# Kernel tuning notes

Hardware: AMD Instinct MI355X
Metric: run time of the kernel (lower is better)

The kernel has to match this reference:

```python
import jax, jax.numpy as jnp
import numpy as np


def setup_inputs() -> dict:
    key = jax.random.key(0)
    ks = jax.random.split(key, 6)
    N, E, F, H, HOP = 100000, 1600000, 128, 128, 3
    x = jax.random.normal(ks[0], (N, F), dtype=jnp.float32)
    edge_index = jax.random.randint(ks[1], (2, E), 0, N, dtype=jnp.int64)
    # per-hop weights, scaled like nn.Linear default init magnitude
    W1 = jax.random.normal(ks[2], (HOP, H, F), dtype=jnp.float32) * (1.0 / np.sqrt(F))
    W2 = jax.random.normal(ks[3], (HOP, H, H), dtype=jnp.float32) * (1.0 / np.sqrt(H))
    W3 = jax.random.normal(ks[4], (HOP, H, H), dtype=jnp.float32) * (1.0 / np.sqrt(H))
    W4 = jax.random.normal(ks[5], (HOP, H, 1), dtype=jnp.float32)
    return {"x": x, "edge_index": edge_index, "W1": W1, "W2": W2, "W3": W3, "W4": W4}


def reference(x, edge_index, W1, W2, W3, W4):
    N = x.shape[0]
    E = edge_index.shape[1]
    H = W1.shape[1]
    hop = W1.shape[0]
    row, col = edge_index[0], edge_index[1]
    edge_attr = jnp.ones((E, 1), dtype=x.dtype)  # as in original forward
    h = jnp.zeros((N, H), dtype=x.dtype)  # initial node_embedding
    for i in range(hop):
        node_feat = x @ W1[i].T                                   # [N,H]
        # gather neighbor embeddings then scatter-sum to destination nodes
        nbr_agg = jax.ops.segment_sum(h[col], row, num_segments=N)  # [N,H]
        edge_emb = jax.nn.relu(edge_attr @ W4[i].T)               # [E,H]
        edge_agg = jax.ops.segment_sum(edge_emb, row, num_segments=N)  # [N,H]
        h = jax.nn.relu(node_feat + nbr_agg @ W2[i].T + edge_agg @ W3[i].T)
        # dropout is identity in eval mode
    return h
```

## Files before the change

### kernel.cpp

```cpp
#include <hip/hip_runtime.h>

#define H 128
#define BSH 9
#define BROWS (1 << BSH)
#define BCAP 10240

typedef __attribute__((ext_vector_type(8))) short bf16x8;
typedef __attribute__((ext_vector_type(4))) float f32x4;
typedef unsigned int uint;
typedef unsigned short ushort;

__device__ __forceinline__ ushort f2bf(float f) {
    uint u = __builtin_bit_cast(uint, f);
    uint r = u + 0x7FFFu + ((u >> 16) & 1u);
    return (ushort)(r >> 16);
}
__device__ __forceinline__ float bf_lo(uint u) {
    return __builtin_bit_cast(float, u << 16);
}
__device__ __forceinline__ float bf_hi(uint u) {
    return __builtin_bit_cast(float, u & 0xFFFF0000u);
}


__global__ void scatter_direct(const int* __restrict__ ei, int E, int NB,
                               int* __restrict__ gcnt, int2* __restrict__ ebuf) {
    __shared__ int cnt[1024];
    __shared__ int base[1024];
    int blk = blockIdx.x, t = threadIdx.x;
    for (int b = t; b < NB; b += 256) cnt[b] = 0;
    __syncthreads();
    int lo = blk << 12, hi = min(lo + 4096, E);
    for (int e = lo + t; e < hi; e += 256) atomicAdd(&cnt[ei[e] >> BSH], 1);
    __syncthreads();
    for (int b = t; b < NB; b += 256) {
        int c = cnt[b];
        base[b] = c ? atomicAdd(&gcnt[b * 16], c) : 0;
        cnt[b] = 0;
    }
    __syncthreads();
    for (int e = lo + t; e < hi; e += 256) {
        int r = ei[e], c = ei[E + e];
        int b = r >> BSH;
        int pos = base[b] + atomicAdd(&cnt[b], 1);
        if (pos < BCAP) ebuf[(size_t)b * BCAP + pos] = make_int2(r, c);
    }
}

__global__ __launch_bounds__(512)
void bucket_csr2(const int2* __restrict__ ebuf, const int* __restrict__ gcnt,
                 int NB, int N, int* __restrict__ deg, int* __restrict__ off,
                 int* __restrict__ colss) {
    __shared__ int rcnt[BROWS], rloff[BROWS];
    int b = blockIdx.x, t = threadIdx.x;
    int rowbase = b << BSH;
    int ebase = b * BCAP;
    int ne = min(gcnt[b * 16], BCAP);
    rcnt[t] = 0;
    __syncthreads();
    for (int e = t; e < ne; e += 512) atomicAdd(&rcnt[ebuf[(size_t)ebase + e].x - rowbase], 1);
    __syncthreads();
    int v = rcnt[t];
    rloff[t] = v;
    __syncthreads();
    for (int d = 1; d < BROWS; d <<= 1) {
        int u = (t >= d) ? rloff[t - d] : 0;
        __syncthreads();
        rloff[t] += u;
        __syncthreads();
    }
    int ex = rloff[t] - v;
    int row = rowbase + t;
    if (row < N) {
        deg[row] = v;
        off[row] = ebase + ex;
    }
    __syncthreads();
    rloff[t] = ex;
    rcnt[t] = 0;
    __syncthreads();
    for (int e = t; e < ne; e += 512) {
        int2 rc = ebuf[(size_t)ebase + e];
        int lr = rc.x - rowbase;
        int pz = atomicAdd(&rcnt[lr], 1);
        colss[ebase + rloff[lr] + pz] = rc.y;
    }
}


__global__ void cvec_kernel(const float* __restrict__ W3, const float* __restrict__ W4,
                            float* __restrict__ cvec) {
    __shared__ float r4[H];
    int i = blockIdx.x, t = threadIdx.x;
    if (t < H) r4[t] = fmaxf(W4[i * H + t], 0.f);
    __syncthreads();
    int wv = t >> 6, l = t & 63;
    for (int k = wv; k < H; k += 4) {
        const float* w3 = W3 + (size_t)i * H * H + (size_t)k * H;
        float s = w3[l] * r4[l] + w3[l + 64] * r4[l + 64];
        for (int d = 1; d < 64; d <<= 1) s += __shfl_xor(s, d);
        if (l == 0) cvec[i * H + k] = s;
    }
}

__global__ void cast_w(const float* __restrict__ W1, const float* __restrict__ W2,
                       ushort* __restrict__ outp, int n8) {
    int i = blockIdx.x * blockDim.x + threadIdx.x;
    if (i >= 2 * n8) return;
    const float4* in4 = (const float4*)((i < n8) ? W1 : W2);
    int j = (i < n8) ? i : i - n8;
    float4 a = in4[2 * j], b = in4[2 * j + 1];
    uint4 o;
    o.x = (uint)f2bf(a.x) | ((uint)f2bf(a.y) << 16);
    o.y = (uint)f2bf(a.z) | ((uint)f2bf(a.w) << 16);
    o.z = (uint)f2bf(b.x) | ((uint)f2bf(b.y) << 16);
    o.w = (uint)f2bf(b.z) | ((uint)f2bf(b.w) << 16);
    ((uint4*)outp)[i] = o;
}


template<int RELU, int OUT_BF16, int CAST0>
__global__ __launch_bounds__(512)
void gemm_pairs(const void* __restrict__ A0, const ushort* __restrict__ W0,
                const ushort* __restrict__ A1, const ushort* __restrict__ W1p,
                int npairs, const int* __restrict__ deg, const float* __restrict__ cvec,
                void* __restrict__ Cout, ushort* __restrict__ xbout, int N)
{
    __shared__ uint4 A4[2048];
    __shared__ uint4 W4[1024];
    int t = threadIdx.x;
    int w = t >> 6, l = t & 63;
    int lg = l >> 4, lr = l & 15;
    int rowBase = blockIdx.x * 256;

    f32x4 acc[2][8];
#pragma unroll
    for (int rt = 0; rt < 2; ++rt)
#pragma unroll
        for (int ct = 0; ct < 8; ++ct) acc[rt][ct] = (f32x4){0.f, 0.f, 0.f, 0.f};

    for (int pr = 0; pr < npairs; ++pr) {
        const uint4* Ag = (const uint4*)(pr ? (const void*)A1 : A0);
        const uint4* Wg = (const uint4*)(pr ? W1p : W0);
        for (int kc = 0; kc < 2; ++kc) {
            if (pr || kc) __syncthreads();
#pragma unroll
            for (int it = 0; it < 4; ++it) {
                int idx = it * 512 + t;
                int r = idx >> 3, s = idx & 7;
                int gr = rowBase + r;
                uint4 v = make_uint4(0, 0, 0, 0);
                if (CAST0 && pr == 0) {
                    if (gr < N) {
                        const float4* xg = (const float4*)A0;
                        float4 a = xg[(size_t)gr * 32 + (kc * 8 + s) * 2];
                        float4 b = xg[(size_t)gr * 32 + (kc * 8 + s) * 2 + 1];
                        v.x = (uint)f2bf(a.x) | ((uint)f2bf(a.y) << 16);
                        v.y = (uint)f2bf(a.z) | ((uint)f2bf(a.w) << 16);
                        v.z = (uint)f2bf(b.x) | ((uint)f2bf(b.y) << 16);
                        v.w = (uint)f2bf(b.z) | ((uint)f2bf(b.w) << 16);
                        ((uint4*)xbout)[(size_t)gr * 16 + kc * 8 + s] = v;
                    }
                } else {
                    if (gr < N) v = Ag[(size_t)gr * 16 + kc * 8 + s];
                }
                A4[r * 8 + (s ^ (r & 7))] = v;
            }
#pragma unroll
            for (int it = 0; it < 2; ++it) {
                int idx = it * 512 + t;
                int r = idx >> 3, s = idx & 7;
                W4[r * 8 + (s ^ (r & 7))] = Wg[r * 16 + kc * 8 + s];
            }
            __syncthreads();
#pragma unroll
            for (int kk = 0; kk < 2; ++kk) {
                int slot = kk * 4 + lg;
                bf16x8 af[2], bfr[8];
#pragma unroll
                for (int rt = 0; rt < 2; ++rt) {
                    int r = w * 32 + rt * 16 + lr;
                    af[rt] = *(const bf16x8*)&A4[r * 8 + (slot ^ (r & 7))];
                }
#pragma unroll
                for (int ct = 0; ct < 8; ++ct) {
                    int r = ct * 16 + lr;
                    bfr[ct] = *(const bf16x8*)&W4[r * 8 + (slot ^ (r & 7))];
                }
#pragma unroll
                for (int rt = 0; rt < 2; ++rt)
#pragma unroll
                    for (int ct = 0; ct < 8; ++ct)
                        acc[rt][ct] = __builtin_amdgcn_mfma_f32_16x16x32_bf16(
                            af[rt], bfr[ct], acc[rt][ct], 0, 0, 0);
            }
        }
    }

    float cv[8];
#pragma unroll
    for (int ct = 0; ct < 8; ++ct) cv[ct] = cvec[ct * 16 + lr];
#pragma unroll
    for (int rt = 0; rt < 2; ++rt) {
#pragma unroll
        for (int j = 0; j < 4; ++j) {
            int gr = rowBase + w * 32 + rt * 16 + lg * 4 + j;
            if (gr < N) {
                float d = (float)deg[gr];
#pragma unroll
                for (int ct = 0; ct < 8; ++ct) {
                    int gc = ct * 16 + lr;
                    float v = acc[rt][ct][j] + d * cv[ct];
                    if (RELU) v = fmaxf(v, 0.f);
                    if (OUT_BF16) ((ushort*)Cout)[(size_t)gr * H + gc] = f2bf(v);
                    else ((float*)Cout)[(size_t)gr * H + gc] = v;
                }
            }
        }
    }
}


__global__ void aggregate_sum(const ushort* __restrict__ hsrc,
                              const int* __restrict__ off, const int* __restrict__ deg,
                              const int* __restrict__ cols,
                              ushort* __restrict__ sdst, int N)
{
    int node = blockIdx.x * 4 + (threadIdx.x >> 6);
    if (node >= N) return;
    int l = threadIdx.x & 63;
    int s = off[node], e = s + deg[node];
    const uint* pu = (const uint*)hsrc;
    float ax = 0.f, ay = 0.f;
    int i = s;
    for (; i + 8 <= e; i += 8) {
        uint v0 = pu[(size_t)cols[i]     * 64 + l];
        uint v1 = pu[(size_t)cols[i + 1] * 64 + l];
        uint v2 = pu[(size_t)cols[i + 2] * 64 + l];
        uint v3 = pu[(size_t)cols[i + 3] * 64 + l];
        uint v4 = pu[(size_t)cols[i + 4] * 64 + l];
        uint v5 = pu[(size_t)cols[i + 5] * 64 + l];
        uint v6 = pu[(size_t)cols[i + 6] * 64 + l];
        uint v7 = pu[(size_t)cols[i + 7] * 64 + l];
        ax += bf_lo(v0) + bf_lo(v1) + bf_lo(v2) + bf_lo(v3)
            + bf_lo(v4) + bf_lo(v5) + bf_lo(v6) + bf_lo(v7);
        ay += bf_hi(v0) + bf_hi(v1) + bf_hi(v2) + bf_hi(v3)
            + bf_hi(v4) + bf_hi(v5) + bf_hi(v6) + bf_hi(v7);
    }
    for (; i + 4 <= e; i += 4) {
        uint v0 = pu[(size_t)cols[i]     * 64 + l];
        uint v1 = pu[(size_t)cols[i + 1] * 64 + l];
        uint v2 = pu[(size_t)cols[i + 2] * 64 + l];
        uint v3 = pu[(size_t)cols[i + 3] * 64 + l];
        ax += bf_lo(v0) + bf_lo(v1) + bf_lo(v2) + bf_lo(v3);
        ay += bf_hi(v0) + bf_hi(v1) + bf_hi(v2) + bf_hi(v3);
    }
    for (; i < e; ++i) {
        uint v = pu[(size_t)cols[i] * 64 + l];
        ax += bf_lo(v);
        ay += bf_hi(v);
    }
    ((uint*)sdst)[(size_t)node * 64 + l] = (uint)f2bf(ax) | ((uint)f2bf(ay) << 16);
}


extern "C" void kernel_launch(void* const* d_in, const int* in_sizes, int n_in,
                              void* d_out, int out_size, void* d_ws, size_t ws_size,
                              hipStream_t stream)
{
    const float* x  = (const float*)d_in[0];
    const int*   ei = (const int*)d_in[1];
    const float* W1 = (const float*)d_in[2];
    const float* W2 = (const float*)d_in[3];
    const float* W3 = (const float*)d_in[4];
    const float* W4 = (const float*)d_in[5];
    int N   = in_sizes[0] / H;
    int E   = in_sizes[1] / 2;
    int HOP = in_sizes[2] / (H * H);

    int NB   = (N + BROWS - 1) >> BSH;
    int NBLK = (E + 4095) >> 12;

    char* ws = (char*)d_ws;
    int*   gcnt  = (int*)ws;
    int*   deg   = gcnt + NB * 16;
    int*   off   = deg + N;
    int*   colss = off + N;
    float* cvec  = (float*)(colss + (size_t)NB * BCAP);
    size_t fo = (((size_t)((char*)(cvec + HOP * H) - ws)) + 255) & ~(size_t)255;
    int2*  ebuf  = (int2*)(ws + fo);
    ushort* W1b  = (ushort*)(ebuf + (size_t)NB * BCAP);
    ushort* W2b  = W1b + (size_t)HOP * H * H;
    ushort* xb   = W2b + (size_t)HOP * H * H;
    ushort* h    = xb + (size_t)N * H;
    ushort* sagg = h + (size_t)N * H;

    hipMemsetAsync(gcnt, 0, sizeof(int) * NB * 16, stream);
    scatter_direct<<<NBLK, 256, 0, stream>>>(ei, E, NB, gcnt, ebuf);
    bucket_csr2<<<NB, 512, 0, stream>>>(ebuf, gcnt, NB, N, deg, off, colss);

    cvec_kernel<<<HOP, 256, 0, stream>>>(W3, W4, cvec);

    int nw8 = HOP * H * H / 8;
    cast_w<<<(2 * nw8 + 255) / 256, 256, 0, stream>>>(W1, W2, W1b, nw8);

    int gblocks = (N + 255) / 256;
    float* out = (float*)d_out;

    if (HOP == 1) {
        gemm_pairs<1, 0, 1><<<gblocks, 512, 0, stream>>>(x, W1b, nullptr, nullptr, 1,
                                                         deg, cvec, out, xb, N);
        return;
    }
    gemm_pairs<1, 1, 1><<<gblocks, 512, 0, stream>>>(x, W1b, nullptr, nullptr, 1,
                                                     deg, cvec, h, xb, N);

    for (int i = 1; i < HOP; ++i) {
        int last = (i == HOP - 1);
        aggregate_sum<<<(N + 3) / 4, 256, 0, stream>>>(h, off, deg, colss, sagg, N);
        if (last)
            gemm_pairs<1, 0, 0><<<gblocks, 512, 0, stream>>>(xb, W1b + (size_t)i * H * H,
                                                             sagg, W2b + (size_t)i * H * H,
                                                             2, deg, cvec + i * H, out,
                                                             nullptr, N);
        else
            gemm_pairs<1, 1, 0><<<gblocks, 512, 0, stream>>>(xb, W1b + (size_t)i * H * H,
                                                             sagg, W2b + (size_t)i * H * H,
                                                             2, deg, cvec + i * H, h,
                                                             nullptr, N);
    }
}
```

Measured before the change: 262.7 us.

## Gather hop-1 neighbor embeddings in FP8 and enlarge CSR buckets

Adds a cast kernel that quantizes the bf16 hidden state to FP8 (scaled by 1/8, clamped to 448) and an FP8 gather-sum kernel for the first aggregation hop. This halves the bytes read per neighbor in that gather, at the cost of an extra cast pass and reduced precision. It also doubles the CSR bucket size (1024 rows, 1024-thread blocks) to cut the number of buckets in the sorting step.

New measurement: 285.0 us. +8.5%, slower.

```diff
diff --git a/kernel.cpp b/kernel.cpp
--- a/kernel.cpp
+++ b/kernel.cpp
@@ -1,14 +1,16 @@
 #include <hip/hip_runtime.h>
 
 #define H 128
-#define BSH 9
+#define BSH 10
 #define BROWS (1 << BSH)
-#define BCAP 10240
+#define BCAP 18432
 
 typedef __attribute__((ext_vector_type(8))) short bf16x8;
 typedef __attribute__((ext_vector_type(4))) float f32x4;
+typedef __attribute__((ext_vector_type(2))) float f32x2;
 typedef unsigned int uint;
 typedef unsigned short ushort;
+typedef unsigned char uchar;
 
 __device__ __forceinline__ ushort f2bf(float f) {
     uint u = __builtin_bit_cast(uint, f);
@@ -20,6 +22,49 @@
 }
 __device__ __forceinline__ float bf_hi(uint u) {
     return __builtin_bit_cast(float, u & 0xFFFF0000u);
+}
+
+
+__device__ __forceinline__ uint fp8_enc1(float v) {
+    if (v < 0.015625f) {
+        float r = v * 512.0f;
+        uint q = (uint)(r + 0.5f);
+        return q > 8u ? 8u : q;
+    }
+    uint u = __builtin_bit_cast(uint, v);
+    u += 0x7FFFFu + ((u >> 20) & 1u);
+    int ef = (int)(u >> 23) - 120;
+    uint r = ((uint)ef << 3) | ((u >> 20) & 7u);
+    if (ef > 15 || r > 0x7Eu) r = 0x7Eu;
+    return r;
+}
+
+__device__ __forceinline__ float2 fp8_dec2(uint v) {
+#if __has_builtin(__builtin_amdgcn_cvt_pk_f32_fp8)
+    f32x2 r = __builtin_amdgcn_cvt_pk_f32_fp8((int)v, false);
+    return make_float2(r[0], r[1]);
+#else
+    float2 o;
+    uint b0 = v & 0xFFu, b1 = (v >> 8) & 0xFFu;
+    uint e0 = (b0 >> 3) & 15u, m0 = b0 & 7u;
+    uint e1 = (b1 >> 3) & 15u, m1 = b1 & 7u;
+    float n0 = __builtin_bit_cast(float, ((e0 + 120u) << 23) | (m0 << 20));
+    float n1 = __builtin_bit_cast(float, ((e1 + 120u) << 23) | (m1 << 20));
+    o.x = e0 ? n0 : (float)m0 * 0.001953125f;
+    o.y = e1 ? n1 : (float)m1 * 0.001953125f;
+    return o;
+#endif
+}
+
+__device__ __forceinline__ uint fp8_enc4(float a, float b, float c, float d) {
+#if __has_builtin(__builtin_amdgcn_cvt_pk_fp8_f32)
+    int w = 0;
+    w = __builtin_amdgcn_cvt_pk_fp8_f32(a, b, w, false);
+    w = __builtin_amdgcn_cvt_pk_fp8_f32(c, d, w, true);
+    return (uint)w;
+#else
+    return fp8_enc1(a) | (fp8_enc1(b) << 8) | (fp8_enc1(c) << 16) | (fp8_enc1(d) << 24);
+#endif
 }
 
 
@@ -47,7 +92,7 @@
     }
 }
 
-__global__ __launch_bounds__(512)
+__global__ __launch_bounds__(1024)
 void bucket_csr2(const int2* __restrict__ ebuf, const int* __restrict__ gcnt,
                  int NB, int N, int* __restrict__ deg, int* __restrict__ off,
                  int* __restrict__ colss) {
@@ -58,7 +103,7 @@
     int ne = min(gcnt[b * 16], BCAP);
     rcnt[t] = 0;
     __syncthreads();
-    for (int e = t; e < ne; e += 512) atomicAdd(&rcnt[ebuf[(size_t)ebase + e].x - rowbase], 1);
+    for (int e = t; e < ne; e += 1024) atomicAdd(&rcnt[ebuf[(size_t)ebase + e].x - rowbase], 1);
     __syncthreads();
     int v = rcnt[t];
     rloff[t] = v;
@@ -79,7 +124,7 @@
     rloff[t] = ex;
     rcnt[t] = 0;
     __syncthreads();
-    for (int e = t; e < ne; e += 512) {
+    for (int e = t; e < ne; e += 1024) {
         int2 rc = ebuf[(size_t)ebase + e];
         int lr = rc.x - rowbase;
         int pz = atomicAdd(&rcnt[lr], 1);
@@ -116,6 +161,20 @@
     o.z = (uint)f2bf(b.x) | ((uint)f2bf(b.y) << 16);
     o.w = (uint)f2bf(b.z) | ((uint)f2bf(b.w) << 16);
     ((uint4*)outp)[i] = o;
+}
+
+__global__ void cast_h8(const ushort* __restrict__ h, uchar* __restrict__ h8, int n8) {
+    int i = blockIdx.x * blockDim.x + threadIdx.x;
+    if (i >= n8) return;
+    uint4 v = ((const uint4*)h)[i];
+    float f0 = fminf(bf_lo(v.x) * 0.125f, 448.f), f1 = fminf(bf_hi(v.x) * 0.125f, 448.f);
+    float f2 = fminf(bf_lo(v.y) * 0.125f, 448.f), f3 = fminf(bf_hi(v.y) * 0.125f, 448.f);
+    float f4 = fminf(bf_lo(v.z) * 0.125f, 448.f), f5 = fminf(bf_hi(v.z) * 0.125f, 448.f);
+    float f6 = fminf(bf_lo(v.w) * 0.125f, 448.f), f7 = fminf(bf_hi(v.w) * 0.125f, 448.f);
+    uint2 o;
+    o.x = fp8_enc4(f0, f1, f2, f3);
+    o.y = fp8_enc4(f4, f5, f6, f7);
+    ((uint2*)h8)[i] = o;
 }
 
 
@@ -264,6 +323,43 @@
 }
 
 
+__global__ void aggregate_fp8(const uchar* __restrict__ h8,
+                              const int* __restrict__ off, const int* __restrict__ deg,
+                              const int* __restrict__ cols,
+                              ushort* __restrict__ sdst, int N)
+{
+    int node = blockIdx.x * 4 + (threadIdx.x >> 6);
+    if (node >= N) return;
+    int l = threadIdx.x & 63;
+    int s = off[node], e = s + deg[node];
+    const ushort* pu = (const ushort*)h8;
+    float ax = 0.f, ay = 0.f;
+    int i = s;
+    for (; i + 8 <= e; i += 8) {
+        uint v0 = pu[(size_t)cols[i]     * 64 + l];
+        uint v1 = pu[(size_t)cols[i + 1] * 64 + l];
+        uint v2 = pu[(size_t)cols[i + 2] * 64 + l];
+        uint v3 = pu[(size_t)cols[i + 3] * 64 + l];
+        uint v4 = pu[(size_t)cols[i + 4] * 64 + l];
+        uint v5 = pu[(size_t)cols[i + 5] * 64 + l];
+        uint v6 = pu[(size_t)cols[i + 6] * 64 + l];
+        uint v7 = pu[(size_t)cols[i + 7] * 64 + l];
+        float2 f0 = fp8_dec2(v0), f1 = fp8_dec2(v1), f2 = fp8_dec2(v2), f3 = fp8_dec2(v3);
+        float2 f4 = fp8_dec2(v4), f5 = fp8_dec2(v5), f6 = fp8_dec2(v6), f7 = fp8_dec2(v7);
+        ax += f0.x + f1.x + f2.x + f3.x + f4.x + f5.x + f6.x + f7.x;
+        ay += f0.y + f1.y + f2.y + f3.y + f4.y + f5.y + f6.y + f7.y;
+    }
+    for (; i < e; ++i) {
+        float2 f = fp8_dec2(pu[(size_t)cols[i] * 64 + l]);
+        ax += f.x;
+        ay += f.y;
+    }
+    ax *= 8.f;
+    ay *= 8.f;
+    ((uint*)sdst)[(size_t)node * 64 + l] = (uint)f2bf(ax) | ((uint)f2bf(ay) << 16);
+}
+
+
 extern "C" void kernel_launch(void* const* d_in, const int* in_sizes, int n_in,
                               void* d_out, int out_size, void* d_ws, size_t ws_size,
                               hipStream_t stream)
@@ -294,10 +390,11 @@
     ushort* xb   = W2b + (size_t)HOP * H * H;
     ushort* h    = xb + (size_t)N * H;
     ushort* sagg = h + (size_t)N * H;
+    uchar*  h8   = (uchar*)(sagg + (size_t)N * H);
 
     hipMemsetAsync(gcnt, 0, sizeof(int) * NB * 16, stream);
     scatter_direct<<<NBLK, 256, 0, stream>>>(ei, E, NB, gcnt, ebuf);
-    bucket_csr2<<<NB, 512, 0, stream>>>(ebuf, gcnt, NB, N, deg, off, colss);
+    bucket_csr2<<<NB, 1024, 0, stream>>>(ebuf, gcnt, NB, N, deg, off, colss);
 
     cvec_kernel<<<HOP, 256, 0, stream>>>(W3, W4, cvec);
 
@@ -315,9 +412,15 @@
     gemm_pairs<1, 1, 1><<<gblocks, 512, 0, stream>>>(x, W1b, nullptr, nullptr, 1,
                                                      deg, cvec, h, xb, N);
 
+    int nh8 = N * H / 8;
     for (int i = 1; i < HOP; ++i) {
         int last = (i == HOP - 1);
-        aggregate_sum<<<(N + 3) / 4, 256, 0, stream>>>(h, off, deg, colss, sagg, N);
+        if (i == 1) {
+            cast_h8<<<(nh8 + 255) / 256, 256, 0, stream>>>(h, h8, nh8);
+            aggregate_fp8<<<(N + 3) / 4, 256, 0, stream>>>(h8, off, deg, colss, sagg, N);
+        } else {
+            aggregate_sum<<<(N + 3) / 4, 256, 0, stream>>>(h, off, deg, colss, sagg, N);
+        }
         if (last)
             gemm_pairs<1, 0, 0><<<gblocks, 512, 0, stream>>>(xb, W1b + (size_t)i * H * H,
                                                              sagg, W2b + (size_t)i * H * H,
```
